# Kernel optimization log

Hardware: AMD Instinct MI355X
Metric: run time of the kernel (lower is better)

The kernel has to match this reference:

```python
import jax, jax.numpy as jnp
import numpy as np

H, D_MODEL, DK, DV = 16, 1024, 64, 64
B, S = 4, 2048
LN_EPS = 1e-6
NEG = -1e9


def setup_inputs() -> dict:
    key = jax.random.key(0)
    ks = jax.random.split(key, 8)
    query = jax.random.normal(ks[0], (B, S, D_MODEL), dtype=jnp.float32)
    k_in = jax.random.normal(ks[1], (B, S, D_MODEL), dtype=jnp.float32)
    v_in = jax.random.normal(ks[2], (B, S, D_MODEL), dtype=jnp.float32)
    mask = jax.random.randint(ks[3], (B, S, S), 0, 2, dtype=jnp.int32)
    sc = 1.0 / np.sqrt(D_MODEL)
    w_qs = jax.random.normal(ks[4], (D_MODEL, H * DK), dtype=jnp.float32) * sc
    w_ks = jax.random.normal(ks[5], (D_MODEL, H * DK), dtype=jnp.float32) * sc
    w_vs = jax.random.normal(ks[6], (D_MODEL, H * DV), dtype=jnp.float32) * sc
    w_out = jax.random.normal(ks[7], (H * DV, D_MODEL), dtype=jnp.float32) * (1.0 / np.sqrt(H * DV))
    ln_g = jnp.ones((D_MODEL,), dtype=jnp.float32)
    ln_b = jnp.zeros((D_MODEL,), dtype=jnp.float32)
    return {"query": query, "key": k_in, "value": v_in, "mask": mask,
            "w_qs": w_qs, "w_ks": w_ks, "w_vs": w_vs, "w_out": w_out,
            "ln_g": ln_g, "ln_b": ln_b}


def reference(query, key, value, mask, w_qs, w_ks, w_vs, w_out, ln_g, ln_b):
    # projections -> [B, H, S, dk/dv]
    q = (query @ w_qs).reshape(B, S, H, DK).transpose(0, 2, 1, 3)
    k = (key @ w_ks).reshape(B, S, H, DK).transpose(0, 2, 1, 3)
    v = (value @ w_vs).reshape(B, S, H, DV).transpose(0, 2, 1, 3)
    scores = jnp.einsum('bhqd,bhkd->bhqk', q, k) / np.sqrt(DK)
    scores = jnp.where(mask[:, None, :, :] == 0, NEG, scores)
    p = jax.nn.softmax(scores, axis=-1)  # dropout = identity in eval
    x = jnp.einsum('bhqk,bhkd->bhqd', p, v)  # [B,H,S,DV]
    x = x.transpose(0, 2, 1, 3).reshape(B, S, H * DV)
    out = x @ w_out + query  # dropout identity, residual
    mu = out.mean(-1, keepdims=True)
    var = out.var(-1, keepdims=True)
    return (out - mu) / jnp.sqrt(var + LN_EPS) * ln_g + ln_b
```

## Files before the change

### kernel.cpp

```cpp
#include <hip/hip_runtime.h>

#define BB   4
#define SS   2048
#define HH   16
#define DM   1024
#define DKV  64
#define LNEPS 1e-6f

#define MD_BF16 0
#define MD_F32  1
#define MD_F16  2

typedef __attribute__((ext_vector_type(8))) short bf16x8;
typedef __attribute__((ext_vector_type(4))) float f32x4;
#define MFMA16(a,b,c) __builtin_amdgcn_mfma_f32_16x16x32_bf16(a,b,c,0,0,0)

__device__ __forceinline__ float2 unpack2(unsigned int u) {
    union { unsigned int i; float f; } a, b;
    a.i = u << 16;
    b.i = u & 0xffff0000u;
    return make_float2(a.f, b.f);
}
__device__ __forceinline__ unsigned short f2bf(float f) {
    union { float f; unsigned int i; } c; c.f = f;
    unsigned int u = c.i;
    unsigned int r = u + 0x7fffu + ((u >> 16) & 1u);
    return (unsigned short)(r >> 16);
}
__device__ __forceinline__ unsigned short f2bf_t(float f) {
    union { float f; unsigned int i; } c; c.f = f;
    return (unsigned short)(c.i >> 16);
}
__device__ __forceinline__ float h2f(unsigned int bits16) {
    unsigned short s = (unsigned short)bits16;
    _Float16 x;
    __builtin_memcpy(&x, &s, 2);
    return (float)x;
}
__device__ __forceinline__ void load8m(const void* p, int mode, size_t e0, float* o) {
    if (mode == MD_F32) {
        const float* f = (const float*)p + e0;
        float4 a = *(const float4*)f;
        float4 b = *(const float4*)(f + 4);
        o[0] = a.x; o[1] = a.y; o[2] = a.z; o[3] = a.w;
        o[4] = b.x; o[5] = b.y; o[6] = b.z; o[7] = b.w;
    } else {
        uint4 u = *(const uint4*)((const ushort*)p + e0);
        unsigned v[4] = {u.x, u.y, u.z, u.w};
        if (mode == MD_BF16) {
#pragma unroll
            for (int j = 0; j < 4; ++j) { float2 t = unpack2(v[j]); o[2*j] = t.x; o[2*j+1] = t.y; }
        } else {
#pragma unroll
            for (int j = 0; j < 4; ++j) { o[2*j] = h2f(v[j] & 0xFFFFu); o[2*j+1] = h2f(v[j] >> 16); }
        }
    }
}
__device__ __forceinline__ void load4m(const void* p, int mode, size_t e0, float* o) {
    if (mode == MD_F32) {
        float4 v = *(const float4*)((const float*)p + e0);
        o[0] = v.x; o[1] = v.y; o[2] = v.z; o[3] = v.w;
    } else {
        uint2 u = *(const uint2*)((const ushort*)p + e0);
        if (mode == MD_BF16) {
            float2 a = unpack2(u.x), b = unpack2(u.y);
            o[0] = a.x; o[1] = a.y; o[2] = b.x; o[3] = b.y;
        } else {
            o[0] = h2f(u.x & 0xFFFFu); o[1] = h2f(u.x >> 16);
            o[2] = h2f(u.y & 0xFFFFu); o[3] = h2f(u.y >> 16);
        }
    }
}
__device__ __forceinline__ float loadS(const void* p, int mode, size_t i) {
    if (mode == MD_F32) return ((const float*)p)[i];
    unsigned short u = ((const ushort*)p)[i];
    if (mode == MD_BF16) { union { unsigned i; float f; } c; c.i = (unsigned)u << 16; return c.f; }
    return h2f(u);
}

struct SniffArgs { const void* p[10]; int nhalf[10]; };

__global__ void sniff_all(SniffArgs a, int* __restrict__ modes) {
    __shared__ int cE, cO;
    const int slots[9] = {0, 1, 2, 4, 5, 6, 7, 8, 9};
    const int slot = slots[blockIdx.x];
    const ushort* p = (const ushort*)a.p[slot];
    const int nhalf = a.nhalf[slot];
    if (threadIdx.x == 0) { cE = 0; cO = 0; }
    __syncthreads();
    int e = 0, o = 0;
    for (int i = threadIdx.x; i < nhalf; i += 256) {
        unsigned ex = (p[i] >> 7) & 0xFFu;
        int hit = (ex < 100u || ex == 0xFFu) ? 1 : 0;
        if (i & 1) o += hit; else e += hit;
    }
    atomicAdd(&cE, e);
    atomicAdd(&cO, o);
    __syncthreads();
    if (threadIdx.x == 0) {
        int total = cE + cO;
        modes[slot] = (total < 48) ? MD_BF16 : ((cO * 4 < cE) ? MD_F32 : MD_F16);
    }
}

__global__ __launch_bounds__(256) void wtrans(
    const void* __restrict__ W, ushort* __restrict__ Wt,
    const int* __restrict__ modes, int wslot)
{
    __shared__ ushort T[64][68];
    const int tid = threadIdx.x;
    const int m = modes[wslot];
    const int k0 = blockIdx.y * 64, n0 = blockIdx.x * 64;

    const int r = tid >> 2, c = (tid & 3) * 16;
    float t[4];
#pragma unroll
    for (int j = 0; j < 4; ++j) {
        load4m(W, m, (size_t)(k0 + r) * DM + n0 + c + 4 * j, t);
#pragma unroll
        for (int i = 0; i < 4; ++i) T[r][c + 4 * j + i] = f2bf(t[i]);
    }
    __syncthreads();

    const int rn = tid >> 2, ck = (tid & 3) * 16;
    union { ushort u[8]; uint4 v; } p0, p1;
#pragma unroll
    for (int j = 0; j < 8; ++j) { p0.u[j] = T[ck + j][rn]; p1.u[j] = T[ck + 8 + j][rn]; }
    ushort* op = &Wt[(size_t)(n0 + rn) * DM + k0 + ck];
    *(uint4*)op = p0.v;
    *(uint4*)(op + 8) = p1.v;
}

__global__ __launch_bounds__(256) void proj_mfma(
    const void* __restrict__ Araw, const ushort* __restrict__ Wt,
    ushort* __restrict__ Out, const int* __restrict__ modes,
    int aslot, int vmode, float scale)
{
    __shared__ __align__(16) ushort As[128][40];
    __shared__ __align__(16) ushort Bs[128][40];

    const int tid = threadIdx.x;
    const int lane = tid & 63, wv = tid >> 6;
    const int quad = lane >> 4, L = lane & 15;
    const int m0 = blockIdx.y * 128, n0 = blockIdx.x * 128;
    const int wm = (wv >> 1) * 64, wn = (wv & 1) * 64;
    const int ma = modes[aslot];

    f32x4 acc[4][4];
#pragma unroll
    for (int i = 0; i < 4; ++i)
#pragma unroll
        for (int j = 0; j < 4; ++j) { acc[i][j][0] = 0.f; acc[i][j][1] = 0.f; acc[i][j][2] = 0.f; acc[i][j][3] = 0.f; }

    const int arow = tid >> 1, aseg = tid & 1;

    for (int kt = 0; kt < 32; ++kt) {
        const int k0 = kt * 32;
        {
            float t0[8], t1[8];
            load8m(Araw, ma, (size_t)(m0 + arow) * DM + k0 + aseg * 16, t0);
            load8m(Araw, ma, (size_t)(m0 + arow) * DM + k0 + aseg * 16 + 8, t1);
            union { ushort u[8]; uint4 v; } p0, p1;
#pragma unroll
            for (int j = 0; j < 8; ++j) { p0.u[j] = f2bf(t0[j]); p1.u[j] = f2bf(t1[j]); }
            *(uint4*)&As[arow][aseg * 16]     = p0.v;
            *(uint4*)&As[arow][aseg * 16 + 8] = p1.v;

            const ushort* wp = &Wt[(size_t)(n0 + arow) * DM + k0 + aseg * 16];
            *(uint4*)&Bs[arow][aseg * 16]     = *(const uint4*)wp;
            *(uint4*)&Bs[arow][aseg * 16 + 8] = *(const uint4*)(wp + 8);
        }
        __syncthreads();

        bf16x8 af[4], bfr[4];
#pragma unroll
        for (int tm = 0; tm < 4; ++tm) af[tm] = *(const bf16x8*)&As[wm + tm * 16 + L][quad * 8];
#pragma unroll
        for (int tn = 0; tn < 4; ++tn) bfr[tn] = *(const bf16x8*)&Bs[wn + tn * 16 + L][quad * 8];
#pragma unroll
        for (int tm = 0; tm < 4; ++tm)
#pragma unroll
            for (int tn = 0; tn < 4; ++tn)
                acc[tm][tn] = MFMA16(af[tm], bfr[tn], acc[tm][tn]);
        __syncthreads();
    }

#pragma unroll
    for (int tm = 0; tm < 4; ++tm)
#pragma unroll
        for (int tn = 0; tn < 4; ++tn)
#pragma unroll
            for (int r = 0; r < 4; ++r) {
                const int mm = m0 + wm + tm * 16 + quad * 4 + r;
                const int n = n0 + wn + tn * 16 + L;
                const int b = mm >> 11, s = mm & 2047;
                const int h = n >> 6, d = n & 63;
                const size_t o = vmode
                    ? ((size_t)(b * HH + h) * DKV + d) * SS + s
                    : ((size_t)(b * HH + h) * SS + s) * DKV + d;
                Out[o] = f2bf(acc[tm][tn][r] * scale);
            }
}

__global__ __launch_bounds__(256) void attn_mfma(
    const ushort* __restrict__ Q, const ushort* __restrict__ K,
    const ushort* __restrict__ Vt, const int* __restrict__ mask,
    ushort* __restrict__ Xo)
{
    __shared__ __align__(16) ushort Ks[64][72];
    __shared__ __align__(16) ushort Vs[64][72];
    __shared__ __align__(16) ushort Ps[64][72];

    const int tid = threadIdx.x;
    const int lane = tid & 63, wv = tid >> 6;
    const int quad = lane >> 4, L = lane & 15;
    const int bh = blockIdx.x, b = bh >> 4, h = bh & 15;
    const int q0 = blockIdx.y * 64;

    const ushort* qp = &Q[((size_t)bh * SS + q0 + wv * 16 + L) * DKV + quad * 8];
    const bf16x8 aq0 = *(const bf16x8*)qp;
    const bf16x8 aq1 = *(const bf16x8*)(qp + 32);

    f32x4 O[4];
    float lacc[4];
#pragma unroll
    for (int t = 0; t < 4; ++t) { O[t][0] = 0.f; O[t][1] = 0.f; O[t][2] = 0.f; O[t][3] = 0.f; }
#pragma unroll
    for (int r = 0; r < 4; ++r) lacc[r] = 0.f;

    const int sr = tid >> 2, sg = tid & 3;
    const ushort* kbase = &K[((size_t)bh * SS + sr) * DKV + sg * 16];
    const ushort* vbase = &Vt[((size_t)bh * DKV + sr) * SS + sg * 16];
    const int* mrow[4];
#pragma unroll
    for (int r = 0; r < 4; ++r)
        mrow[r] = &mask[((size_t)b * SS + q0 + wv * 16 + quad * 4 + r) * SS + L];

    for (int kt = 0; kt < 32; ++kt) {
        __syncthreads();
        *(uint4*)&Ks[sr][sg * 16]     = *(const uint4*)kbase;
        *(uint4*)&Ks[sr][sg * 16 + 8] = *(const uint4*)(kbase + 8);
        *(uint4*)&Vs[sr][sg * 16]     = *(const uint4*)vbase;
        *(uint4*)&Vs[sr][sg * 16 + 8] = *(const uint4*)(vbase + 8);
        kbase += 64 * DKV;
        vbase += 64;
        __syncthreads();

        f32x4 sc[4];
#pragma unroll
        for (int t = 0; t < 4; ++t) {
            bf16x8 b0 = *(const bf16x8*)&Ks[t * 16 + L][quad * 8];
            bf16x8 b1 = *(const bf16x8*)&Ks[t * 16 + L][32 + quad * 8];
            f32x4 c; c[0] = 0.f; c[1] = 0.f; c[2] = 0.f; c[3] = 0.f;
            c = MFMA16(aq0, b0, c);
            c = MFMA16(aq1, b1, c);
            sc[t] = c;
        }

#pragma unroll
        for (int r = 0; r < 4; ++r) {
            const int* mp = mrow[r] + kt * 64;
#pragma unroll
            for (int t = 0; t < 4; ++t) {
                const float s = fminf(sc[t][r], 30.f);
                const float e = __expf(s);
                const float p = mp[t * 16] ? e : 0.f;
                lacc[r] += p;
                Ps[wv * 16 + quad * 4 + r][t * 16 + L] = f2bf_t(p);
            }
        }

        bf16x8 ap0 = *(const bf16x8*)&Ps[wv * 16 + L][quad * 8];
        bf16x8 ap1 = *(const bf16x8*)&Ps[wv * 16 + L][32 + quad * 8];
#pragma unroll
        for (int t = 0; t < 4; ++t) {
            bf16x8 v0 = *(const bf16x8*)&Vs[t * 16 + L][quad * 8];
            bf16x8 v1 = *(const bf16x8*)&Vs[t * 16 + L][32 + quad * 8];
            O[t] = MFMA16(ap0, v0, O[t]);
            O[t] = MFMA16(ap1, v1, O[t]);
        }
    }

    float inv[4];
#pragma unroll
    for (int r = 0; r < 4; ++r) {
        float l = lacc[r];
#pragma unroll
        for (int off = 1; off < 16; off <<= 1) l += __shfl_xor(l, off, 64);
        inv[r] = 1.f / l;
    }
#pragma unroll
    for (int t = 0; t < 4; ++t)
#pragma unroll
        for (int r = 0; r < 4; ++r) {
            const int qg = q0 + wv * 16 + quad * 4 + r;
            Xo[((size_t)b * SS + qg) * DM + h * DKV + t * 16 + L] = f2bf(O[t][r] * inv[r]);
        }
}

__global__ __launch_bounds__(256) void oproj_mfma(
    const ushort* __restrict__ Xin, const ushort* __restrict__ Wt,
    const void* __restrict__ Qres, float* __restrict__ Out,
    const int* __restrict__ modes)
{
    __shared__ __align__(16) ushort As[128][40];
    __shared__ __align__(16) ushort Bs[128][40];

    const int tid = threadIdx.x;
    const int lane = tid & 63, wv = tid >> 6;
    const int quad = lane >> 4, L = lane & 15;
    const int m0 = blockIdx.y * 128, n0 = blockIdx.x * 128;
    const int wm = (wv >> 1) * 64, wn = (wv & 1) * 64;
    const int mq = modes[0];

    f32x4 acc[4][4];
#pragma unroll
    for (int i = 0; i < 4; ++i)
#pragma unroll
        for (int j = 0; j < 4; ++j) { acc[i][j][0] = 0.f; acc[i][j][1] = 0.f; acc[i][j][2] = 0.f; acc[i][j][3] = 0.f; }

    const int arow = tid >> 1, aseg = tid & 1;

    for (int kt = 0; kt < 32; ++kt) {
        const int k0 = kt * 32;
        {
            const ushort* xp = &Xin[(size_t)(m0 + arow) * DM + k0 + aseg * 16];
            *(uint4*)&As[arow][aseg * 16]     = *(const uint4*)xp;
            *(uint4*)&As[arow][aseg * 16 + 8] = *(const uint4*)(xp + 8);
            const ushort* wp = &Wt[(size_t)(n0 + arow) * DM + k0 + aseg * 16];
            *(uint4*)&Bs[arow][aseg * 16]     = *(const uint4*)wp;
            *(uint4*)&Bs[arow][aseg * 16 + 8] = *(const uint4*)(wp + 8);
        }
        __syncthreads();

        bf16x8 af[4], bfr[4];
#pragma unroll
        for (int tm = 0; tm < 4; ++tm) af[tm] = *(const bf16x8*)&As[wm + tm * 16 + L][quad * 8];
#pragma unroll
        for (int tn = 0; tn < 4; ++tn) bfr[tn] = *(const bf16x8*)&Bs[wn + tn * 16 + L][quad * 8];
#pragma unroll
        for (int tm = 0; tm < 4; ++tm)
#pragma unroll
            for (int tn = 0; tn < 4; ++tn)
                acc[tm][tn] = MFMA16(af[tm], bfr[tn], acc[tm][tn]);
        __syncthreads();
    }

#pragma unroll
    for (int tm = 0; tm < 4; ++tm)
#pragma unroll
        for (int tn = 0; tn < 4; ++tn)
#pragma unroll
            for (int r = 0; r < 4; ++r) {
                const int mm = m0 + wm + tm * 16 + quad * 4 + r;
                const int n = n0 + wn + tn * 16 + L;
                const size_t idx = (size_t)mm * DM + n;
                Out[idx] = acc[tm][tn][r] + loadS(Qres, mq, idx);
            }
}

__global__ __launch_bounds__(256) void ln_k(
    float* __restrict__ Out, const void* __restrict__ G,
    const void* __restrict__ Bt, const int* __restrict__ modes)
{
    const int tid = threadIdx.x, wv = tid >> 6, lane = tid & 63;
    const int row = blockIdx.x * 4 + wv;
    const int mg = modes[8], mb = modes[9];
    const size_t base = (size_t)row * DM + lane * 16;

    float v[16];
    float s = 0.f, q = 0.f;
#pragma unroll
    for (int j = 0; j < 16; j += 4) {
        float4 t = *(const float4*)&Out[base + j];
        v[j] = t.x; v[j+1] = t.y; v[j+2] = t.z; v[j+3] = t.w;
        s += t.x + t.y + t.z + t.w;
        q += t.x*t.x + t.y*t.y + t.z*t.z + t.w*t.w;
    }
#pragma unroll
    for (int off = 1; off < 64; off <<= 1) {
        s += __shfl_xor(s, off, 64);
        q += __shfl_xor(q, off, 64);
    }
    const float mu = s * (1.f / 1024.f);
    const float var = q * (1.f / 1024.f) - mu * mu;
    const float inv = rsqrtf(var + LNEPS);

    float gj[16], bj[16];
#pragma unroll
    for (int j = 0; j < 16; j += 4) {
        load4m(G,  mg, (size_t)lane * 16 + j, gj + j);
        load4m(Bt, mb, (size_t)lane * 16 + j, bj + j);
    }
#pragma unroll
    for (int j = 0; j < 16; j += 4) {
        float4 o;
        o.x = (v[j]   - mu) * inv * gj[j]   + bj[j];
        o.y = (v[j+1] - mu) * inv * gj[j+1] + bj[j+1];
        o.z = (v[j+2] - mu) * inv * gj[j+2] + bj[j+2];
        o.w = (v[j+3] - mu) * inv * gj[j+3] + bj[j+3];
        *(float4*)&Out[base + j] = o;
    }
}

extern "C" void kernel_launch(void* const* d_in, const int* in_sizes, int n_in,
                              void* d_out, int out_size, void* d_ws, size_t ws_size,
                              hipStream_t stream)
{
    const void* query = d_in[0];
    const void* key_i = d_in[1];
    const void* value = d_in[2];
    const int*  mask  = (const int*)d_in[3];
    const void* w_qs  = d_in[4];
    const void* w_ks  = d_in[5];
    const void* w_vs  = d_in[6];
    const void* w_out = d_in[7];
    const void* ln_g  = d_in[8];
    const void* ln_b  = d_in[9];
    float* out = (float*)d_out;

    int* modes = (int*)d_ws;
    const size_t PE = (size_t)BB * HH * SS * DKV;
    ushort* Qw = (ushort*)((char*)d_ws + 256);
    ushort* Kw = Qw + PE;
    ushort* Vw = Kw + PE;
    ushort* Xw = Vw + PE;
    ushort* Wt  = Xw;
    ushort* Wt2 = Qw;

    SniffArgs sa;
    for (int i = 0; i < 10; ++i) {
        sa.p[i] = d_in[i];
        sa.nhalf[i] = in_sizes[i] < 4096 ? in_sizes[i] : 4096;
    }
    sniff_all<<<9, 256, 0, stream>>>(sa, modes);

    dim3 gproj(8, 64), gtr(16, 16);

    wtrans<<<gtr, 256, 0, stream>>>(w_qs, Wt, modes, 4);
    proj_mfma<<<gproj, 256, 0, stream>>>(query, Wt, Qw, modes, 0, 0, 0.125f);
    wtrans<<<gtr, 256, 0, stream>>>(w_ks, Wt, modes, 5);
    proj_mfma<<<gproj, 256, 0, stream>>>(key_i, Wt, Kw, modes, 1, 0, 1.0f);
    wtrans<<<gtr, 256, 0, stream>>>(w_vs, Wt, modes, 6);
    proj_mfma<<<gproj, 256, 0, stream>>>(value, Wt, Vw, modes, 2, 1, 1.0f);

    attn_mfma<<<dim3(64, 32), 256, 0, stream>>>(Qw, Kw, Vw, mask, Xw);

    wtrans<<<gtr, 256, 0, stream>>>(w_out, Wt2, modes, 7);
    oproj_mfma<<<gproj, 256, 0, stream>>>(Xw, Wt2, query, out, modes);
    ln_k<<<2048, 256, 0, stream>>>(out, ln_g, ln_b, modes);
}
```

Before: 604.0 us.

## Pack int32 attention mask into bitmask and reorder attention grid

Adds a pre-pass kernel that compresses the int32 mask into one bit per element, stored in the output buffer as scratch. The attention kernel then reads 32-bit mask words instead of int32s, cutting the mask traffic that every head previously re-read from the full B×S×S int array. The grid is also transposed so blocks for the same head run close together. The extra pack pass reads the full mask once and relies on the output buffer being free until the output projection writes it.

```diff
diff --git a/kernel.cpp b/kernel.cpp
--- a/kernel.cpp
+++ b/kernel.cpp
@@ -103,6 +103,23 @@
     }
 }
 
+__global__ __launch_bounds__(256) void mpack(
+    const int* __restrict__ mask, unsigned int* __restrict__ pm)
+{
+    const int w = blockIdx.x * 256 + threadIdx.x;
+    const int* p = mask + (size_t)w * 32;
+    unsigned int bits = 0u;
+#pragma unroll
+    for (int j = 0; j < 8; ++j) {
+        int4 v = *(const int4*)(p + j * 4);
+        bits |= (v.x ? 1u : 0u) << (4 * j);
+        bits |= (v.y ? 1u : 0u) << (4 * j + 1);
+        bits |= (v.z ? 1u : 0u) << (4 * j + 2);
+        bits |= (v.w ? 1u : 0u) << (4 * j + 3);
+    }
+    pm[w] = bits;
+}
+
 __global__ __launch_bounds__(256) void wtrans(
     const void* __restrict__ W, ushort* __restrict__ Wt,
     const int* __restrict__ modes, int wslot)
@@ -204,7 +221,7 @@
 
 __global__ __launch_bounds__(256) void attn_mfma(
     const ushort* __restrict__ Q, const ushort* __restrict__ K,
-    const ushort* __restrict__ Vt, const int* __restrict__ mask,
+    const ushort* __restrict__ Vt, const unsigned int* __restrict__ pm,
     ushort* __restrict__ Xo)
 {
     __shared__ __align__(16) ushort Ks[64][72];
@@ -214,8 +231,8 @@
     const int tid = threadIdx.x;
     const int lane = tid & 63, wv = tid >> 6;
     const int quad = lane >> 4, L = lane & 15;
-    const int bh = blockIdx.x, b = bh >> 4, h = bh & 15;
-    const int q0 = blockIdx.y * 64;
+    const int bh = blockIdx.y, b = bh >> 4, h = bh & 15;
+    const int q0 = blockIdx.x * 64;
 
     const ushort* qp = &Q[((size_t)bh * SS + q0 + wv * 16 + L) * DKV + quad * 8];
     const bf16x8 aq0 = *(const bf16x8*)qp;
@@ -231,10 +248,10 @@
     const int sr = tid >> 2, sg = tid & 3;
     const ushort* kbase = &K[((size_t)bh * SS + sr) * DKV + sg * 16];
     const ushort* vbase = &Vt[((size_t)bh * DKV + sr) * SS + sg * 16];
-    const int* mrow[4];
+    const unsigned int* pmr[4];
 #pragma unroll
     for (int r = 0; r < 4; ++r)
-        mrow[r] = &mask[((size_t)b * SS + q0 + wv * 16 + quad * 4 + r) * SS + L];
+        pmr[r] = pm + ((size_t)b * SS + q0 + wv * 16 + quad * 4 + r) * 64;
 
     for (int kt = 0; kt < 32; ++kt) {
         __syncthreads();
@@ -244,6 +261,11 @@
         *(uint4*)&Vs[sr][sg * 16 + 8] = *(const uint4*)(vbase + 8);
         kbase += 64 * DKV;
         vbase += 64;
+
+        uint2 mw[4];
+#pragma unroll
+        for (int r = 0; r < 4; ++r) mw[r] = *(const uint2*)(pmr[r] + 2 * kt);
+
         __syncthreads();
 
         f32x4 sc[4];
@@ -259,12 +281,13 @@
 
 #pragma unroll
         for (int r = 0; r < 4; ++r) {
-            const int* mp = mrow[r] + kt * 64;
+            const unsigned mx = mw[r].x, my = mw[r].y;
 #pragma unroll
             for (int t = 0; t < 4; ++t) {
                 const float s = fminf(sc[t][r], 30.f);
                 const float e = __expf(s);
-                const float p = mp[t * 16] ? e : 0.f;
+                const unsigned wsel = (t & 2) ? my : mx;
+                const float p = ((wsel >> ((t & 1) * 16 + L)) & 1u) ? e : 0.f;
                 lacc[r] += p;
                 Ps[wv * 16 + quad * 4 + r][t * 16 + L] = f2bf_t(p);
             }
@@ -427,6 +450,7 @@
     ushort* Xw = Vw + PE;
     ushort* Wt  = Xw;
     ushort* Wt2 = Qw;
+    unsigned int* pmask = (unsigned int*)d_out;
 
     SniffArgs sa;
     for (int i = 0; i < 10; ++i) {
@@ -434,6 +458,7 @@
         sa.nhalf[i] = in_sizes[i] < 4096 ? in_sizes[i] : 4096;
     }
     sniff_all<<<9, 256, 0, stream>>>(sa, modes);
+    mpack<<<2048, 256, 0, stream>>>(mask, pmask);
 
     dim3 gproj(8, 64), gtr(16, 16);
 
@@ -444,7 +469,7 @@
     wtrans<<<gtr, 256, 0, stream>>>(w_vs, Wt, modes, 6);
     proj_mfma<<<gproj, 256, 0, stream>>>(value, Wt, Vw, modes, 2, 1, 1.0f);
 
-    attn_mfma<<<dim3(64, 32), 256, 0, stream>>>(Qw, Kw, Vw, mask, Xw);
+    attn_mfma<<<dim3(32, 64), 256, 0, stream>>>(Qw, Kw, Vw, pmask, Xw);
 
     wtrans<<<gtr, 256, 0, stream>>>(w_out, Wt2, modes, 7);
     oproj_mfma<<<gproj, 256, 0, stream>>>(Xw, Wt2, query, out, modes);
```

After: 586.5 us. 1.03x faster.
